# Kernel optimization log

Hardware: AMD Instinct MI355X
Metric: run time of the kernel (lower is better)

The kernel has to match this reference:

```python
import jax, jax.numpy as jnp
import numpy as np

N_HEADS = 16
D_EMBD = 1024
B, T = 2, 2048


def setup_inputs() -> dict:
    key = jax.random.key(0)
    k1, k2, k3 = jax.random.split(key, 3)
    x = jax.random.normal(k1, (B, T, D_EMBD), dtype=jnp.float32)
    W1 = jax.random.normal(k2, (D_EMBD, 3 * D_EMBD), dtype=jnp.float32) / np.sqrt(D_EMBD)
    b1 = jnp.zeros((3 * D_EMBD,), dtype=jnp.float32)
    W2 = jax.random.normal(k3, (D_EMBD, D_EMBD), dtype=jnp.float32) / np.sqrt(D_EMBD)
    b2 = jnp.zeros((D_EMBD,), dtype=jnp.float32)
    return {"x": x, "W1": W1, "b1": b1, "W2": W2, "b2": b2}


def reference(x, W1, b1, W2, b2):
    bs, t, d = x.shape
    h = N_HEADS
    kqv = x @ W1 + b1  # [b, t, 3d]
    # note original split order: k, q, v
    k, q, v = jnp.split(kqv, 3, axis=-1)
    # [b, t, d] -> [b, h, t, dh]
    def to_heads(z):
        return z.reshape(bs, t, h, d // h).transpose(0, 2, 1, 3)
    k, q, v = to_heads(k), to_heads(q), to_heads(v)
    mask = jnp.tril(jnp.ones((t, t), dtype=bool))
    attn = jnp.where(mask, jnp.einsum('bhqd,bhkd->bhqk', q, k), 0.0)  # softmax-free retention
    out = jnp.einsum('bhqk,bhkd->bhqd', attn, v)
    out = out.transpose(0, 2, 1, 3).reshape(bs, t, d)  # [b, t, d]
    return out @ W2 + b2
```

## Files before the change

### kernel.cpp

```cpp
#include <hip/hip_runtime.h>
#include <hip/hip_bf16.h>

typedef __bf16 bf16x8 __attribute__((ext_vector_type(8)));
typedef float f32x4 __attribute__((ext_vector_type(4)));
typedef float f32x16 __attribute__((ext_vector_type(16)));
typedef unsigned short ushort_t;
typedef unsigned short ushort8 __attribute__((ext_vector_type(8)));
typedef unsigned int uint4v __attribute__((ext_vector_type(4)));


__device__ inline void gload_lds16(const void* g, void* l) {
  __builtin_amdgcn_global_load_lds(
      (const __attribute__((address_space(1))) void*)g,
      (__attribute__((address_space(3))) void*)l, 16, 0, 0);
}

__device__ inline ushort_t f2bf(float f) {
  unsigned int u = __float_as_uint(f);
  unsigned int lsb = (u >> 16) & 1u;
  u += 0x7fffu + lsb;
  return (ushort_t)(u >> 16);
}


__global__ __launch_bounds__(256) void f32_to_bf16_vec(
    const float* __restrict__ in, ushort_t* __restrict__ out) {
  int i = (blockIdx.x * 256 + threadIdx.x) * 8;
  float4 a = *(const float4*)&in[i];
  float4 b = *(const float4*)&in[i + 4];
  ushort8 o;
  o[0] = f2bf(a.x); o[1] = f2bf(a.y); o[2] = f2bf(a.z); o[3] = f2bf(a.w);
  o[4] = f2bf(b.x); o[5] = f2bf(b.y); o[6] = f2bf(b.z); o[7] = f2bf(b.w);
  *(ushort8*)&out[i] = o;
}

__global__ __launch_bounds__(256) void transpose_f32_bf16(
    const float* __restrict__ in, ushort_t* __restrict__ out, int R, int C) {
  __shared__ float tile[32][33];
  const int tx = threadIdx.x & 31, ty = threadIdx.x >> 5;
  const int c0 = blockIdx.x * 32, r0 = blockIdx.y * 32;
#pragma unroll
  for (int i = 0; i < 32; i += 8)
    tile[ty + i][tx] = in[(size_t)(r0 + ty + i) * C + c0 + tx];
  __syncthreads();
#pragma unroll
  for (int i = 0; i < 32; i += 8)
    out[(size_t)(c0 + ty + i) * R + r0 + tx] = f2bf(tile[tx][ty + i]);
}

__global__ __launch_bounds__(256) void transpose_v(
    const ushort_t* __restrict__ kqv, ushort_t* __restrict__ vt) {
  __shared__ ushort_t tile[64 * 64];
  const int tt = blockIdx.x;
  const int bh = blockIdx.y;
  const int b = bh >> 4, h = bh & 15;
  const int tid = threadIdx.x;
#pragma unroll
  for (int p = 0; p < 2; p++) {
    const int tr = (tid >> 3) + p * 32;
    const int c8 = tid & 7;
    ushort8 v = *(const ushort8*)&kqv[(size_t)(b * 2048 + tt * 64 + tr) * 3072 +
                                      2048 + h * 64 + c8 * 8];
    *(ushort8*)&tile[tr * 64 + ((c8 ^ (tr & 7)) * 8)] = v;
  }
  __syncthreads();
  const int d = tid & 63;
#pragma unroll
  for (int p = 0; p < 2; p++) {
    const int t8 = (tid >> 6) + p * 4;
    ushort8 o;
#pragma unroll
    for (int j = 0; j < 8; j++) {
      const int t = t8 * 8 + j;
      o[j] = tile[t * 64 + (((d >> 3) ^ (t & 7)) * 8) + (d & 7)];
    }
    *(ushort8*)&vt[(size_t)(bh * 64 + d) * 2048 + tt * 64 + t8 * 8] = o;
  }
}


template <bool OUT_BF16>
__global__ __launch_bounds__(256) void gemm_bt(
    const ushort_t* __restrict__ A, const ushort_t* __restrict__ BT,
    const float* __restrict__ bias, void* __restrict__ Cout,
    int M, int N, int K) {
  __shared__ ushort_t lA[128 * 32];
  __shared__ ushort_t lB[128 * 32];
  const int tid = threadIdx.x;
  const int lane = tid & 63;
  const int wave = tid >> 6;
  const int wr = wave >> 1, wc = wave & 1;
  const int l16 = lane & 15, lhi = lane >> 4;
  const int bx = blockIdx.x, by = blockIdx.y;

  const ushort_t* gA = A + (size_t)(by * 128 + (tid >> 2)) * K + (tid & 3) * 8;
  const ushort_t* gB = BT + (size_t)(bx * 128 + (tid >> 2)) * K + (tid & 3) * 8;

  f32x4 acc[4][4] = {};

  for (int k0 = 0; k0 < K; k0 += 32) {
    gload_lds16(gA + k0, &lA[tid * 8]);
    gload_lds16(gA + k0 + (size_t)64 * K, &lA[tid * 8 + 2048]);
    gload_lds16(gB + k0, &lB[tid * 8]);
    gload_lds16(gB + k0 + (size_t)64 * K, &lB[tid * 8 + 2048]);
    __syncthreads();

    bf16x8 af[4], bfr[4];
#pragma unroll
    for (int m = 0; m < 4; m++)
      af[m] = *(const bf16x8*)&lA[(wr * 64 + m * 16 + l16) * 32 + lhi * 8];
#pragma unroll
    for (int n = 0; n < 4; n++)
      bfr[n] = *(const bf16x8*)&lB[(wc * 64 + n * 16 + l16) * 32 + lhi * 8];
#pragma unroll
    for (int m = 0; m < 4; m++)
#pragma unroll
      for (int n = 0; n < 4; n++)
        acc[m][n] = __builtin_amdgcn_mfma_f32_16x16x32_bf16(af[m], bfr[n],
                                                            acc[m][n], 0, 0, 0);
    __syncthreads();
  }

  const int r0 = by * 128 + wr * 64 + lhi * 4;
  const int c0 = bx * 128 + wc * 64 + l16;
#pragma unroll
  for (int m = 0; m < 4; m++)
#pragma unroll
    for (int n = 0; n < 4; n++) {
      const int col = c0 + n * 16;
      const float bv = bias[col];
#pragma unroll
      for (int j = 0; j < 4; j++) {
        const int row = r0 + m * 16 + j;
        const float v = acc[m][n][j] + bv;
        if (OUT_BF16)
          ((ushort_t*)Cout)[(size_t)row * N + col] = f2bf(v);
        else
          ((float*)Cout)[(size_t)row * N + col] = v;
      }
    }
}


__global__ __launch_bounds__(256) void attn_kernel(
    const ushort_t* __restrict__ kqv, const ushort_t* __restrict__ vt,
    ushort_t* __restrict__ ao) {
  __shared__ ushort_t lK[2][64 * 64];
  __shared__ ushort_t lVT[2][64 * 64];
  const int tid = threadIdx.x, lane = tid & 63, wave = tid >> 6;
  const int q_rel = lane & 31, hi = lane >> 5;
  const int qs = wave & 1, kb = wave >> 1;
  const int L = blockIdx.x;
  const int xcd = L & 7, t = L >> 3;
  const int bh = xcd * 4 + (t >> 5);
  const int qj = 31 - ((t + bh * 7) & 31);
  const int b = bh >> 4, h = bh & 15;
  const ushort_t* base = kqv + (size_t)b * 2048 * 3072;
  const ushort_t* vbase = vt + (size_t)bh * 64 * 2048;

  size_t kg[2], vg[2];
  int ld[2];
#pragma unroll
  for (int p = 0; p < 2; p++) {
    const int slot = tid + p * 256;
    const int srow = slot >> 3;
    const int scb = (((slot & 7) * 16) ^ ((srow & 7) << 4)) >> 1;
    kg[p] = (size_t)srow * 3072 + h * 64 + scb;
    vg[p] = (size_t)srow * 2048 + scb;
    ld[p] = slot * 8;
  }

  const int wq0 = qj * 64 + qs * 32;
  bf16x8 qf[4];
#pragma unroll
  for (int ds = 0; ds < 4; ds++)
    qf[ds] = *(const bf16x8*)&base[(size_t)(wq0 + q_rel) * 3072 + 1024 + h * 64 +
                                   ds * 16 + hi * 8];

  f32x16 oacc[2] = {};
  const int nkt = qj + 1;

#pragma unroll
  for (int p = 0; p < 2; p++) {
    gload_lds16(&base[kg[p]], &lK[0][ld[p]]);
    gload_lds16(&vbase[vg[p]], &lVT[0][ld[p]]);
  }

  int cur = 0;
  for (int kt = 0; kt < nkt; ++kt) {
    asm volatile("s_waitcnt vmcnt(0)" ::: "memory");
    __builtin_amdgcn_s_barrier();
    asm volatile("" ::: "memory");

    if (kt + 1 < nkt) {
#pragma unroll
      for (int p = 0; p < 2; p++) {
        gload_lds16(&base[(size_t)(kt + 1) * 64 * 3072 + kg[p]], &lK[cur ^ 1][ld[p]]);
        gload_lds16(&vbase[(size_t)(kt + 1) * 64 + vg[p]], &lVT[cur ^ 1][ld[p]]);
      }
    }

    const int kv0 = kt * 64 + kb * 32;
    if (kv0 <= wq0 + 31) {
      f32x16 st = {};
      const int krow = kb * 32 + q_rel;
      const int ksw = krow & 7;
#pragma unroll
      for (int ds = 0; ds < 4; ds++) {
        bf16x8 kf = *(const bf16x8*)&lK[cur][krow * 64 + (((ds * 2 + hi) ^ ksw) * 8)];
        st = __builtin_amdgcn_mfma_f32_32x32x16_bf16(kf, qf[ds], st, 0, 0, 0);
      }
      if (kv0 + 31 > wq0) {
#pragma unroll
        for (int r = 0; r < 16; r++) {
          const int kgl = kv0 + (r & 3) + 8 * (r >> 2) + 4 * hi;
          if (kgl > wq0 + q_rel) st[r] = 0.f;
        }
      }
      unsigned int w0, w1, w2, w3, w4, w5, w6, w7;
      {
        float e0 = st[0], e1 = st[1], e2 = st[2], e3 = st[3];
        float e4 = st[4], e5 = st[5], e6 = st[6], e7 = st[7];
        float e8 = st[8], e9 = st[9], e10 = st[10], e11 = st[11];
        float e12 = st[12], e13 = st[13], e14 = st[14], e15 = st[15];
        asm("v_cvt_pk_bf16_f32 %0, %1, %2" : "=v"(w0) : "v"(e0), "v"(e1));
        asm("v_cvt_pk_bf16_f32 %0, %1, %2" : "=v"(w1) : "v"(e2), "v"(e3));
        asm("v_cvt_pk_bf16_f32 %0, %1, %2" : "=v"(w2) : "v"(e4), "v"(e5));
        asm("v_cvt_pk_bf16_f32 %0, %1, %2" : "=v"(w3) : "v"(e6), "v"(e7));
        asm("v_cvt_pk_bf16_f32 %0, %1, %2" : "=v"(w4) : "v"(e8), "v"(e9));
        asm("v_cvt_pk_bf16_f32 %0, %1, %2" : "=v"(w5) : "v"(e10), "v"(e11));
        asm("v_cvt_pk_bf16_f32 %0, %1, %2" : "=v"(w6) : "v"(e12), "v"(e13));
        asm("v_cvt_pk_bf16_f32 %0, %1, %2" : "=v"(w7) : "v"(e14), "v"(e15));
      }
      asm("v_permlane32_swap_b32 %0, %1" : "+v"(w0), "+v"(w2));
      asm("v_permlane32_swap_b32 %0, %1" : "+v"(w1), "+v"(w3));
      asm("v_permlane32_swap_b32 %0, %1" : "+v"(w4), "+v"(w6));
      asm("v_permlane32_swap_b32 %0, %1" : "+v"(w5), "+v"(w7));
      uint4v u0 = {w0, w1, w2, w3};
      uint4v u1 = {w4, w5, w6, w7};
      bf16x8 pa0 = __builtin_bit_cast(bf16x8, u0);
      bf16x8 pa1 = __builtin_bit_cast(bf16x8, u1);
#pragma unroll
      for (int dt = 0; dt < 2; dt++) {
        const int vrow = dt * 32 + q_rel;
        const int vsw = vrow & 7;
        bf16x8 vf0 = *(const bf16x8*)&lVT[cur][vrow * 64 + (((kb * 4 + hi) ^ vsw) * 8)];
        bf16x8 vf1 = *(const bf16x8*)&lVT[cur][vrow * 64 + (((kb * 4 + 2 + hi) ^ vsw) * 8)];
        oacc[dt] = __builtin_amdgcn_mfma_f32_32x32x16_bf16(pa0, vf0, oacc[dt], 0, 0, 0);
        oacc[dt] = __builtin_amdgcn_mfma_f32_32x32x16_bf16(pa1, vf1, oacc[dt], 0, 0, 0);
      }
    }

    cur ^= 1;
  }

  __syncthreads();
  float* red = (float*)&lK[0][0];
  if (kb == 1) {
#pragma unroll
    for (int dt = 0; dt < 2; dt++)
#pragma unroll
      for (int r = 0; r < 16; r++)
        red[qs * 2048 + (dt * 16 + r) * 64 + lane] = oacc[dt][r];
  }
  __syncthreads();
  if (kb == 0) {
#pragma unroll
    for (int dt = 0; dt < 2; dt++)
#pragma unroll
      for (int r = 0; r < 16; r++) {
        const float v = oacc[dt][r] + red[qs * 2048 + (dt * 16 + r) * 64 + lane];
        const int q = (r & 3) + 8 * (r >> 2) + 4 * hi;
        const int row = wq0 + q;
        const int col = h * 64 + dt * 32 + q_rel;
        ao[(size_t)(b * 2048 + row) * 1024 + col] = f2bf(v);
      }
  }
}


extern "C" void kernel_launch(void* const* d_in, const int* in_sizes, int n_in,
                              void* d_out, int out_size, void* d_ws, size_t ws_size,
                              hipStream_t stream) {
  const float* x  = (const float*)d_in[0];
  const float* W1 = (const float*)d_in[1];
  const float* b1 = (const float*)d_in[2];
  const float* W2 = (const float*)d_in[3];
  const float* b2 = (const float*)d_in[4];
  float* out = (float*)d_out;

  char* ws = (char*)d_ws;
  ushort_t* xb  = (ushort_t*)(ws);
  ushort_t* w1t = (ushort_t*)(ws + 8388608);
  ushort_t* w2t = (ushort_t*)(ws + 14680064);
  ushort_t* kqv = (ushort_t*)(ws + 16777216);
  ushort_t* ao  = (ushort_t*)(ws + 41943040);
  ushort_t* vtb = (ushort_t*)(ws);

  f32_to_bf16_vec<<<2048, 256, 0, stream>>>(x, xb);
  transpose_f32_bf16<<<dim3(96, 32), 256, 0, stream>>>(W1, w1t, 1024, 3072);
  transpose_f32_bf16<<<dim3(32, 32), 256, 0, stream>>>(W2, w2t, 1024, 1024);
  gemm_bt<true ><<<dim3(24, 32), 256, 0, stream>>>(xb, w1t, b1, kqv, 4096, 3072, 1024);
  transpose_v<<<dim3(32, 32), 256, 0, stream>>>(kqv, vtb);
  attn_kernel<<<dim3(1024), 256, 0, stream>>>(kqv, vtb, ao);
  gemm_bt<false><<<dim3(8, 32), 256, 0, stream>>>(ao, w2t, b2, out, 4096, 1024, 1024);
}
```

Measured before the change: 199.2 us.

## Triple-buffer GEMM LDS loads with swizzle and merge prep kernels

Replaces the single-buffered GEMM mainloop with a three-stage LDS ring that prefetches two K-tiles ahead. It uses explicit vmcnt waits and one barrier per iteration, and XOR-swizzles the LDS chunk layout to reduce bank conflicts. The three preprocessing kernels (x cast and the two weight transposes) are merged into one launch to cut launch overhead. Exchanges for triple the LDS footprint, which can lower occupancy, and relies on hand-written waitcnt counts being correct.

Measured after the change: 187.0 us. 1.07x faster.

```diff
diff --git a/kernel.cpp b/kernel.cpp
--- a/kernel.cpp
+++ b/kernel.cpp
@@ -23,22 +23,12 @@
 }
 
 
-__global__ __launch_bounds__(256) void f32_to_bf16_vec(
-    const float* __restrict__ in, ushort_t* __restrict__ out) {
-  int i = (blockIdx.x * 256 + threadIdx.x) * 8;
-  float4 a = *(const float4*)&in[i];
-  float4 b = *(const float4*)&in[i + 4];
-  ushort8 o;
-  o[0] = f2bf(a.x); o[1] = f2bf(a.y); o[2] = f2bf(a.z); o[3] = f2bf(a.w);
-  o[4] = f2bf(b.x); o[5] = f2bf(b.y); o[6] = f2bf(b.z); o[7] = f2bf(b.w);
-  *(ushort8*)&out[i] = o;
-}
-
-__global__ __launch_bounds__(256) void transpose_f32_bf16(
-    const float* __restrict__ in, ushort_t* __restrict__ out, int R, int C) {
+__device__ inline void transpose_tile_f32_bf16(
+    const float* __restrict__ in, ushort_t* __restrict__ out,
+    int R, int C, int cx, int ry, int tid) {
   __shared__ float tile[32][33];
-  const int tx = threadIdx.x & 31, ty = threadIdx.x >> 5;
-  const int c0 = blockIdx.x * 32, r0 = blockIdx.y * 32;
+  const int tx = tid & 31, ty = tid >> 5;
+  const int c0 = cx * 32, r0 = ry * 32;
 #pragma unroll
   for (int i = 0; i < 32; i += 8)
     tile[ty + i][tx] = in[(size_t)(r0 + ty + i) * C + c0 + tx];
@@ -46,6 +36,29 @@
 #pragma unroll
   for (int i = 0; i < 32; i += 8)
     out[(size_t)(c0 + ty + i) * R + r0 + tx] = f2bf(tile[tx][ty + i]);
+}
+
+__global__ __launch_bounds__(256) void prep_kernel(
+    const float* __restrict__ x, const float* __restrict__ W1,
+    const float* __restrict__ W2, ushort_t* __restrict__ xb,
+    ushort_t* __restrict__ w1t, ushort_t* __restrict__ w2t) {
+  const int bid = blockIdx.x;
+  const int tid = threadIdx.x;
+  if (bid < 2048) {
+    int i = (bid * 256 + tid) * 8;
+    float4 a = *(const float4*)&x[i];
+    float4 b = *(const float4*)&x[i + 4];
+    ushort8 o;
+    o[0] = f2bf(a.x); o[1] = f2bf(a.y); o[2] = f2bf(a.z); o[3] = f2bf(a.w);
+    o[4] = f2bf(b.x); o[5] = f2bf(b.y); o[6] = f2bf(b.z); o[7] = f2bf(b.w);
+    *(ushort8*)&xb[i] = o;
+  } else if (bid < 2048 + 3072) {
+    const int t = bid - 2048;
+    transpose_tile_f32_bf16(W1, w1t, 1024, 3072, t % 96, t / 96, tid);
+  } else {
+    const int t = bid - 5120;
+    transpose_tile_f32_bf16(W2, w2t, 1024, 1024, t % 32, t / 32, tid);
+  }
 }
 
 __global__ __launch_bounds__(256) void transpose_v(
@@ -84,8 +97,8 @@
     const ushort_t* __restrict__ A, const ushort_t* __restrict__ BT,
     const float* __restrict__ bias, void* __restrict__ Cout,
     int M, int N, int K) {
-  __shared__ ushort_t lA[128 * 32];
-  __shared__ ushort_t lB[128 * 32];
+  __shared__ ushort_t lA[3][128 * 32];
+  __shared__ ushort_t lB[3][128 * 32];
   const int tid = threadIdx.x;
   const int lane = tid & 63;
   const int wave = tid >> 6;
@@ -93,33 +106,57 @@
   const int l16 = lane & 15, lhi = lane >> 4;
   const int bx = blockIdx.x, by = blockIdx.y;
 
-  const ushort_t* gA = A + (size_t)(by * 128 + (tid >> 2)) * K + (tid & 3) * 8;
-  const ushort_t* gB = BT + (size_t)(bx * 128 + (tid >> 2)) * K + (tid & 3) * 8;
+  const int srow = tid >> 2;
+  const int schunk = (tid & 3) ^ (srow & 3);
+  const ushort_t* gA = A + (size_t)(by * 128 + srow) * K + schunk * 8;
+  const ushort_t* gB = BT + (size_t)(bx * 128 + srow) * K + schunk * 8;
+
+#define GSTAGE(buf, k0)                                            \
+  do {                                                             \
+    gload_lds16(gA + (k0), &lA[buf][tid * 8]);                     \
+    gload_lds16(gA + (k0) + (size_t)64 * K, &lA[buf][tid * 8 + 2048]); \
+    gload_lds16(gB + (k0), &lB[buf][tid * 8]);                     \
+    gload_lds16(gB + (k0) + (size_t)64 * K, &lB[buf][tid * 8 + 2048]); \
+  } while (0)
 
   f32x4 acc[4][4] = {};
-
-  for (int k0 = 0; k0 < K; k0 += 32) {
-    gload_lds16(gA + k0, &lA[tid * 8]);
-    gload_lds16(gA + k0 + (size_t)64 * K, &lA[tid * 8 + 2048]);
-    gload_lds16(gB + k0, &lB[tid * 8]);
-    gload_lds16(gB + k0 + (size_t)64 * K, &lB[tid * 8 + 2048]);
-    __syncthreads();
+  const int NK = K >> 5;
+
+  GSTAGE(0, 0);
+  GSTAGE(1, 32);
+
+  int cur = 0;
+  for (int kt = 0; kt < NK; ++kt) {
+    if (kt + 1 < NK) asm volatile("s_waitcnt vmcnt(4)" ::: "memory");
+    else             asm volatile("s_waitcnt vmcnt(0)" ::: "memory");
+    __builtin_amdgcn_s_barrier();
+    asm volatile("" ::: "memory");
+
+    if (kt + 2 < NK) {
+      const int pf = (cur + 2 >= 3) ? cur - 1 : cur + 2;
+      GSTAGE(pf, (kt + 2) * 32);
+    }
 
     bf16x8 af[4], bfr[4];
 #pragma unroll
-    for (int m = 0; m < 4; m++)
-      af[m] = *(const bf16x8*)&lA[(wr * 64 + m * 16 + l16) * 32 + lhi * 8];
-#pragma unroll
-    for (int n = 0; n < 4; n++)
-      bfr[n] = *(const bf16x8*)&lB[(wc * 64 + n * 16 + l16) * 32 + lhi * 8];
+    for (int m = 0; m < 4; m++) {
+      const int row = wr * 64 + m * 16 + l16;
+      af[m] = *(const bf16x8*)&lA[cur][row * 32 + ((lhi ^ (row & 3)) * 8)];
+    }
+#pragma unroll
+    for (int n = 0; n < 4; n++) {
+      const int row = wc * 64 + n * 16 + l16;
+      bfr[n] = *(const bf16x8*)&lB[cur][row * 32 + ((lhi ^ (row & 3)) * 8)];
+    }
 #pragma unroll
     for (int m = 0; m < 4; m++)
 #pragma unroll
       for (int n = 0; n < 4; n++)
         acc[m][n] = __builtin_amdgcn_mfma_f32_16x16x32_bf16(af[m], bfr[n],
                                                             acc[m][n], 0, 0, 0);
-    __syncthreads();
-  }
+    cur = (cur + 1 >= 3) ? 0 : cur + 1;
+  }
+#undef GSTAGE
 
   const int r0 = by * 128 + wr * 64 + lhi * 4;
   const int c0 = bx * 128 + wc * 64 + l16;
@@ -297,9 +334,7 @@
   ushort_t* ao  = (ushort_t*)(ws + 41943040);
   ushort_t* vtb = (ushort_t*)(ws);
 
-  f32_to_bf16_vec<<<2048, 256, 0, stream>>>(x, xb);
-  transpose_f32_bf16<<<dim3(96, 32), 256, 0, stream>>>(W1, w1t, 1024, 3072);
-  transpose_f32_bf16<<<dim3(32, 32), 256, 0, stream>>>(W2, w2t, 1024, 1024);
+  prep_kernel<<<6144, 256, 0, stream>>>(x, W1, W2, xb, w1t, w2t);
   gemm_bt<true ><<<dim3(24, 32), 256, 0, stream>>>(xb, w1t, b1, kqv, 4096, 3072, 1024);
   transpose_v<<<dim3(32, 32), 256, 0, stream>>>(kqv, vtb);
   attn_kernel<<<dim3(1024), 256, 0, stream>>>(kqv, vtb, ao);
```
